# Kernel tuning notes

Measured on AMD Instinct MI355X. Metric: run time of the kernel, lower is better.

The kernel has to match this reference:

```python
import jax, jax.numpy as jnp
import numpy as np

N_CODES = 4096
D = 256


def setup_inputs() -> dict:
    key = jax.random.key(0)
    k_v, k_w = jax.random.split(key)
    v = jax.random.normal(k_v, (8, 2048, D), dtype=jnp.float32)
    # Embedding init ~ N(0,1), then softmax over dim=1, then row 0 set to 1/d (empty feature)
    w = jax.random.normal(k_w, (N_CODES, D), dtype=jnp.float32)
    w = jax.nn.softmax(w, axis=1)
    w = w.at[0].set(1.0 / D)
    return {"v": v, "vectors": w}


def reference(v, vectors):
    n, d = vectors.shape
    cb = vectors[1:]  # exclude the fixed empty feature at index 0
    # ||v - c||^2 = ||v||^2 - 2 v.c + ||c||^2  (avoids [..., n, d] intermediate)
    v2 = jnp.sum(v * v, axis=-1, keepdims=True)              # [..., 1]
    c2 = jnp.sum(cb * cb, axis=-1)                           # [n-1]
    diff = v2 - 2.0 * jnp.einsum('...d,nd->...n', v, cb) + c2  # [..., n-1]
    idx = jnp.argmin(diff, axis=-1) + 1                      # [...]
    # empty-feature mask: any component differs from 1/d
    mask = jnp.any(v != (1.0 / d), axis=-1)
    idx = jnp.where(mask, idx, 0)
    out = vectors[idx]                                       # gather == onehot @ vectors
    loss = jnp.mean(jnp.square(out - jax.lax.stop_gradient(v)))
    used = jnp.array(0, dtype=jnp.int32)  # eval mode: usage pool is empty
    return out, idx, loss, used
```

## Files before the change

### kernel.cpp

```cpp
#include <hip/hip_runtime.h>
#include <hip/hip_fp16.h>
#include <math.h>
#include <stdint.h>


#define M_TOTAL 16384
#define NCODES  4096
#define D_DIM   256

#define OUT_OFF_IDX  (M_TOTAL * D_DIM)
#define OUT_OFF_LOSS (OUT_OFF_IDX + M_TOTAL)

typedef _Float16 half8 __attribute__((ext_vector_type(8)));
typedef float    float16v __attribute__((ext_vector_type(16)));

__device__ __forceinline__ void gload_lds16(const void* g, void* l) {
  __builtin_amdgcn_global_load_lds(
      (const __attribute__((address_space(1))) void*)g,
      (__attribute__((address_space(3))) void*)l, 16, 0, 0);
}

__global__ __launch_bounds__(256) void prep_kernel(
    const float* __restrict__ V, const float* __restrict__ W,
    _Float16* __restrict__ Vp, _Float16* __restrict__ Bp,
    float* __restrict__ v2, float* __restrict__ c2,
    uint64_t* __restrict__ pk)
{
  __shared__ float T[16 * 264];
  const int t = threadIdx.x;
  const int rloc = t >> 4, seg = t & 15;
  const bool isW = blockIdx.x < 256;
  const int bid2 = isW ? blockIdx.x : (blockIdx.x - 256);
  const int row = bid2 * 16 + rloc;
  const float* X = isW ? W : V;

  if (!isW && bid2 < 64) pk[bid2 * 256 + t] = ~0ULL;

  const float* src = X + (size_t)row * D_DIM + seg * 16;
  float4 x[4];
#pragma unroll
  for (int u = 0; u < 4; ++u) x[u] = ((const float4*)src)[u];
  union { half8 v; _Float16 e[8]; } uh[2], ul[2];
#pragma unroll
  for (int u = 0; u < 4; ++u) {
    float e4[4] = {x[u].x, x[u].y, x[u].z, x[u].w};
#pragma unroll
    for (int j = 0; j < 4; ++j) {
      const int e = u * 4 + j;
      float s = e4[j] * 1024.0f;
      _Float16 h = (_Float16)s;
      uh[e >> 3].e[e & 7] = h;
      ul[e >> 3].e[e & 7] = (_Float16)(s - (float)h);
    }
    *(float4*)&T[rloc * 264 + seg * 16 + u * 4] = x[u];
  }
  if (isW) {
    const int panel = row >> 5, nin = row & 31;
    _Float16* dst = Bp + ((size_t)panel * 16 + seg) * 2048 + nin * 8;
#pragma unroll
    for (int lh = 0; lh < 2; ++lh) {
      *(half8*)(dst + lh * 256)        = uh[lh].v;
      *(half8*)(dst + 1024 + lh * 256) = ul[lh].v;
    }
  } else {
    _Float16* dst = Vp + ((size_t)(row >> 5) * 16 + seg) * 1024 + (row & 31) * 8;
#pragma unroll
    for (int lh = 0; lh < 2; ++lh) {
      *(half8*)(dst + lh * 256)        = uh[lh].v;
      *(half8*)(dst + 512 + lh * 256)  = ul[lh].v;
    }
  }
  __syncthreads();
  const int half = (t >> 3) & 1, j = t & 7;
  const float* tr = &T[rloc * 264 + half * 128 + j];
  float r = __fmul_rn(tr[0], tr[0]);
#pragma unroll
  for (int i = 1; i < 16; ++i) { float e = tr[8 * i]; r = __fadd_rn(r, __fmul_rn(e, e)); }
  r = __fadd_rn(r, __shfl_xor(r, 1));
  r = __fadd_rn(r, __shfl_xor(r, 2));
  r = __fadd_rn(r, __shfl_xor(r, 4));
  r = __fadd_rn(r, __shfl_xor(r, 8));
  if ((t & 15) == 0) { if (isW) c2[row] = r; else v2[row] = r; }
}

__global__ __launch_bounds__(256, 2) void vq_mfma_kernel(
    const _Float16* __restrict__ Vp, const _Float16* __restrict__ Bp,
    const float* __restrict__ v2, const float* __restrict__ c2,
    uint64_t* __restrict__ pk)
{
  __shared__ __align__(16) char smem[77824];
  uint64_t* red2 = (uint64_t*)(smem + 73728);

  const int tid  = threadIdx.x;
  const int lane = tid & 63;
  const int wave = tid >> 6;
  const int wr = wave >> 1, wc = wave & 1;
  const int l31 = lane & 31, lhi = lane >> 5;

  const int bid = blockIdx.x;
  const int xcd  = bid & 7;
  const int seq  = bid >> 3;
  const int mblk = xcd * 8 + (seq & 7);
  const int pblk = seq >> 3;
  const int m0 = mblk * 256;
  const int n0 = pblk * 128;

  const char* gsrc[6];
  int gstr[6], dstOff[6];
#pragma unroll
  for (int j = 0; j < 6; ++j) {
    const int c = wave * 6 + j;
    dstOff[j] = c * 1024;
    if (c < 16) {
      const int p = c >> 1, pl = c & 1;
      gsrc[j] = (const char*)Vp + ((size_t)(mblk * 8 + p) * 16) * 2048 + pl * 1024 + lane * 16;
      gstr[j] = 2048;
    } else {
      const int b = c - 16, pn = b >> 1, pl = b & 1;
      gsrc[j] = (const char*)Bp + ((size_t)(pblk * 4 + pn) * 16) * 4096 + pl * 2048 + lane * 16;
      gstr[j] = 4096;
    }
  }

  auto STAGE = [&](int kb) {
#pragma unroll
    for (int j = 0; j < 6; ++j) {
      gload_lds16(gsrc[j], smem + kb * 24576 + dstOff[j]);
      gsrc[j] += gstr[j];
    }
  };

  float16v acc[4][2];
#pragma unroll
  for (int mb = 0; mb < 4; ++mb)
#pragma unroll
    for (int nb = 0; nb < 2; ++nb) acc[mb][nb] = (float16v)0.0f;

  STAGE(0);
  STAGE(1);

#pragma unroll
  for (int k = 0; k < 16; ++k) {
    if (k < 15) asm volatile("s_waitcnt vmcnt(6)" ::: "memory");
    else        asm volatile("s_waitcnt vmcnt(0)" ::: "memory");
    __builtin_amdgcn_sched_barrier(0);
    __builtin_amdgcn_s_barrier();
    __builtin_amdgcn_sched_barrier(0);
    if (k < 14) STAGE((k + 2) % 3);

    const char* Ab = smem + (k % 3) * 24576 + (wr * 4) * 2048 + lane * 16;
    const char* Bb = smem + (k % 3) * 24576 + 16384 + (wc * 2) * 2048 + lane * 16;
    half8 ah[4], al[4], bh[2], bl[2];
#pragma unroll
    for (int mb = 0; mb < 4; ++mb) {
      ah[mb] = *(const half8*)(Ab + mb * 2048);
      al[mb] = *(const half8*)(Ab + mb * 2048 + 1024);
    }
#pragma unroll
    for (int nb = 0; nb < 2; ++nb) {
      bh[nb] = *(const half8*)(Bb + nb * 2048);
      bl[nb] = *(const half8*)(Bb + nb * 2048 + 1024);
    }
#pragma unroll
    for (int nb = 0; nb < 2; ++nb)
#pragma unroll
      for (int mb = 0; mb < 4; ++mb)
        acc[mb][nb] = __builtin_amdgcn_mfma_f32_32x32x16_f16(ah[mb], bh[nb], acc[mb][nb], 0, 0, 0);
#pragma unroll
    for (int nb = 0; nb < 2; ++nb)
#pragma unroll
      for (int mb = 0; mb < 4; ++mb)
        acc[mb][nb] = __builtin_amdgcn_mfma_f32_32x32x16_f16(ah[mb], bl[nb], acc[mb][nb], 0, 0, 0);
#pragma unroll
    for (int nb = 0; nb < 2; ++nb)
#pragma unroll
      for (int mb = 0; mb < 4; ++mb)
        acc[mb][nb] = __builtin_amdgcn_mfma_f32_32x32x16_f16(al[mb], bh[nb], acc[mb][nb], 0, 0, 0);
  }
  __syncthreads();

  float c2r[2];
#pragma unroll
  for (int nb = 0; nb < 2; ++nb) c2r[nb] = c2[n0 + wc * 64 + nb * 32 + l31];

  uint64_t* wbuf = (uint64_t*)smem + wave * 1056;

#pragma unroll
  for (int mb = 0; mb < 4; ++mb) {
#pragma unroll
    for (int r = 0; r < 16; ++r) {
      const int rowin = (r & 3) + 8 * (r >> 2) + 4 * lhi;
      const float v2m = v2[m0 + wr * 128 + mb * 32 + rowin];
      uint64_t b = ~0ULL;
#pragma unroll
      for (int nb = 0; nb < 2; ++nb) {
        const int n = n0 + wc * 64 + nb * 32 + l31;
        float dot = acc[mb][nb][r] * 0x1p-20f;
        float dd  = __fadd_rn(__fsub_rn(v2m, 2.0f * dot), c2r[nb]);
        if (n == 0) dd = INFINITY;
        uint64_t p = ((uint64_t)__float_as_uint(dd) << 32) | (uint32_t)n;
        if (p < b) b = p;
      }
      wbuf[(r * 2 + lhi) * 33 + l31] = b;
    }
    {
      const int f = lane >> 1, hf = lane & 1;
      const uint64_t* rp = wbuf + f * 33 + hf * 16;
      uint64_t m = rp[0];
#pragma unroll
      for (int i = 1; i < 16; ++i) { uint64_t v = rp[i]; if (v < m) m = v; }
      uint64_t o = __shfl_xor((unsigned long long)m, 1);
      if (o < m) m = o;
      if (hf == 0) {
        const int r_ = f >> 1, lh2 = f & 1;
        const int rowin = (r_ & 3) + 8 * (r_ >> 2) + 4 * lh2;
        red2[(wr * 128 + mb * 32 + rowin) * 2 + wc] = m;
      }
    }
  }
  __syncthreads();

  uint64_t a0 = red2[tid * 2], a1 = red2[tid * 2 + 1];
  atomicMin((unsigned long long*)&pk[m0 + tid], (unsigned long long)(a0 < a1 ? a0 : a1));
}

__global__ __launch_bounds__(256) void gather_kernel(
    const float* __restrict__ V, const float* __restrict__ W,
    const uint64_t* __restrict__ pk,
    float* __restrict__ out, float* __restrict__ outIdx,
    float* __restrict__ lossPartial)
{
  const int q = blockIdx.x * 4 + (threadIdx.x >> 6);
  const int l = threadIdx.x & 63;
  const uint64_t b = pk[q];
  float4 vv = *(const float4*)(V + (size_t)q * D_DIM + l * 4);
  const float inv = 0.00390625f;
  bool ne = (vv.x != inv) | (vv.y != inv) | (vv.z != inv) | (vv.w != inv);
  const int idx = __ballot(ne) ? (int)(uint32_t)b : 0;
  float4 o4 = *(const float4*)(W + (size_t)idx * D_DIM + l * 4);
  *(float4*)(out + (size_t)q * D_DIM + l * 4) = o4;
  if (l == 0) outIdx[q] = (float)idx;
  float dx = o4.x - vv.x, dy = o4.y - vv.y, dz = o4.z - vv.z, dw = o4.w - vv.w;
  float s = dx * dx + dy * dy + dz * dz + dw * dw;
#pragma unroll
  for (int off = 32; off; off >>= 1) s += __shfl_xor(s, off);
  if (l == 0) lossPartial[q] = s;
}

__global__ __launch_bounds__(256) void finalize_kernel(
    const float* __restrict__ lossPartial, float* __restrict__ out)
{
  const int t = threadIdx.x;
  __shared__ float red[256];
  float s = 0.0f;
  for (int i = t; i < M_TOTAL; i += 256) s += lossPartial[i];
  red[t] = s;
  __syncthreads();
  for (int st = 128; st > 0; st >>= 1) {
    if (t < st) red[t] += red[t + st];
    __syncthreads();
  }
  if (t == 0) {
    out[0] = (float)((double)red[0] / (double)(M_TOTAL * D_DIM));
    out[1] = 0.0f;
  }
}

extern "C" void kernel_launch(void* const* d_in, const int* in_sizes, int n_in,
                              void* d_out, int out_size, void* d_ws, size_t ws_size,
                              hipStream_t stream) {
  const float* V = (const float*)d_in[0];
  const float* W = (const float*)d_in[1];
  float* out = (float*)d_out;

  _Float16* Vp = (_Float16*)d_out;

  char* ws = (char*)d_ws;
  _Float16* Bp  = (_Float16*)(ws);
  float*    c2  = (float*)(ws + 8388608);
  float*    v2  = (float*)(ws + 8388608 + 16384);
  uint64_t* pk  = (uint64_t*)(ws + 8388608 + 16384 + 65536);
  float* lossPartial = (float*)(ws + 8388608 + 16384 + 65536 + 131072);

  prep_kernel<<<1280, 256, 0, stream>>>(V, W, Vp, Bp, v2, c2, pk);
  vq_mfma_kernel<<<2048, 256, 0, stream>>>(Vp, Bp, v2, c2, pk);
  gather_kernel<<<M_TOTAL / 4, 256, 0, stream>>>(V, W, pk, out, out + OUT_OFF_IDX, lossPartial);
  finalize_kernel<<<1, 256, 0, stream>>>(lossPartial, out + OUT_OFF_LOSS);
}
```

Measured before the change: 199.2 us.

## Double-buffer LDS fragment reads in registers to overlap with MFMA chain

Adds a register-level ping-pong so the A/B fragments for k-step k+1 are read from LDS while the MFMAs for step k run. The global-to-LDS stage issue, wait and barrier are reordered to fit this schedule. Occupancy in launch bounds drops from 2 to 1 block per CU so the extra fragment registers fit without spilling. This trades fewer resident waves for latency hiding, and the barrier before reading buffer k+1 must still guard against a stage overwriting it.

```diff
diff --git a/kernel.cpp b/kernel.cpp
--- a/kernel.cpp
+++ b/kernel.cpp
@@ -83,7 +83,7 @@
   if ((t & 15) == 0) { if (isW) c2[row] = r; else v2[row] = r; }
 }
 
-__global__ __launch_bounds__(256, 2) void vq_mfma_kernel(
+__global__ __launch_bounds__(256, 1) void vq_mfma_kernel(
     const _Float16* __restrict__ Vp, const _Float16* __restrict__ Bp,
     const float* __restrict__ v2, const float* __restrict__ c2,
     uint64_t* __restrict__ pk)
@@ -136,46 +136,60 @@
 #pragma unroll
     for (int nb = 0; nb < 2; ++nb) acc[mb][nb] = (float16v)0.0f;
 
+  half8 ah[2][4], al[2][4], bh[2][2], bl[2][2];
+
+  auto LDREAD = [&](int kst, int pb) {
+    const char* Ab = smem + (kst % 3) * 24576 + (wr * 4) * 2048 + lane * 16;
+    const char* Bb = smem + (kst % 3) * 24576 + 16384 + (wc * 2) * 2048 + lane * 16;
+#pragma unroll
+    for (int mb = 0; mb < 4; ++mb) {
+      ah[pb][mb] = *(const half8*)(Ab + mb * 2048);
+      al[pb][mb] = *(const half8*)(Ab + mb * 2048 + 1024);
+    }
+#pragma unroll
+    for (int nb = 0; nb < 2; ++nb) {
+      bh[pb][nb] = *(const half8*)(Bb + nb * 2048);
+      bl[pb][nb] = *(const half8*)(Bb + nb * 2048 + 1024);
+    }
+  };
+
   STAGE(0);
   STAGE(1);
+  asm volatile("s_waitcnt vmcnt(6)" ::: "memory");
+  __builtin_amdgcn_sched_barrier(0);
+  __builtin_amdgcn_s_barrier();
+  __builtin_amdgcn_sched_barrier(0);
+  LDREAD(0, 0);
+  __builtin_amdgcn_sched_barrier(0);
 
 #pragma unroll
   for (int k = 0; k < 16; ++k) {
-    if (k < 15) asm volatile("s_waitcnt vmcnt(6)" ::: "memory");
-    else        asm volatile("s_waitcnt vmcnt(0)" ::: "memory");
-    __builtin_amdgcn_sched_barrier(0);
-    __builtin_amdgcn_s_barrier();
-    __builtin_amdgcn_sched_barrier(0);
-    if (k < 14) STAGE((k + 2) % 3);
-
-    const char* Ab = smem + (k % 3) * 24576 + (wr * 4) * 2048 + lane * 16;
-    const char* Bb = smem + (k % 3) * 24576 + 16384 + (wc * 2) * 2048 + lane * 16;
-    half8 ah[4], al[4], bh[2], bl[2];
-#pragma unroll
-    for (int mb = 0; mb < 4; ++mb) {
-      ah[mb] = *(const half8*)(Ab + mb * 2048);
-      al[mb] = *(const half8*)(Ab + mb * 2048 + 1024);
-    }
-#pragma unroll
-    for (int nb = 0; nb < 2; ++nb) {
-      bh[nb] = *(const half8*)(Bb + nb * 2048);
-      bl[nb] = *(const half8*)(Bb + nb * 2048 + 1024);
+    const int pb = k & 1;
+    if (k <= 13) STAGE((k + 2) % 3);
+    if (k <= 13)      asm volatile("s_waitcnt vmcnt(6)" ::: "memory");
+    else if (k == 14) asm volatile("s_waitcnt vmcnt(0)" ::: "memory");
+    if (k < 15) {
+      __builtin_amdgcn_sched_barrier(0);
+      __builtin_amdgcn_s_barrier();
+      __builtin_amdgcn_sched_barrier(0);
+      LDREAD(k + 1, pb ^ 1);
+      __builtin_amdgcn_sched_barrier(0);
     }
 #pragma unroll
     for (int nb = 0; nb < 2; ++nb)
 #pragma unroll
       for (int mb = 0; mb < 4; ++mb)
-        acc[mb][nb] = __builtin_amdgcn_mfma_f32_32x32x16_f16(ah[mb], bh[nb], acc[mb][nb], 0, 0, 0);
+        acc[mb][nb] = __builtin_amdgcn_mfma_f32_32x32x16_f16(ah[pb][mb], bh[pb][nb], acc[mb][nb], 0, 0, 0);
 #pragma unroll
     for (int nb = 0; nb < 2; ++nb)
 #pragma unroll
       for (int mb = 0; mb < 4; ++mb)
-        acc[mb][nb] = __builtin_amdgcn_mfma_f32_32x32x16_f16(ah[mb], bl[nb], acc[mb][nb], 0, 0, 0);
+        acc[mb][nb] = __builtin_amdgcn_mfma_f32_32x32x16_f16(ah[pb][mb], bl[pb][nb], acc[mb][nb], 0, 0, 0);
 #pragma unroll
     for (int nb = 0; nb < 2; ++nb)
 #pragma unroll
       for (int mb = 0; mb < 4; ++mb)
-        acc[mb][nb] = __builtin_amdgcn_mfma_f32_32x32x16_f16(al[mb], bh[nb], acc[mb][nb], 0, 0, 0);
+        acc[mb][nb] = __builtin_amdgcn_mfma_f32_32x32x16_f16(al[pb][mb], bh[pb][nb], acc[mb][nb], 0, 0, 0);
   }
   __syncthreads();
 
```

After: 204.8 us. 2.8% more time.

## Interleave LDS reads, async global loads and MFMA phases with priority hints

Applied to the files above, without the earlier changes.

Restructures the main k-loop so LDS fragment reads, async global-to-LDS staging and the three MFMA groups run in three interleaved phases instead of loading everything up front. The barrier moves to the end of each iteration, and s_setprio raises wave priority around the MFMA bursts. The aim is to hide LDS and global load latency behind matrix math and to keep the MFMA unit busy across waves. It adds extra lgkmcnt waits and scheduling barriers, which could serialize work if the phases are too small.

```diff
diff --git a/kernel.cpp b/kernel.cpp
--- a/kernel.cpp
+++ b/kernel.cpp
@@ -122,10 +122,17 @@
     }
   }
 
-  auto STAGE = [&](int kb) {
+  auto STAGE2 = [&](int kst, int j0) {
+#pragma unroll
+    for (int j = j0; j < j0 + 2; ++j) {
+      gload_lds16(gsrc[j], smem + (kst % 3) * 24576 + dstOff[j]);
+      gsrc[j] += gstr[j];
+    }
+  };
+  auto STAGEFULL = [&](int kst) {
 #pragma unroll
     for (int j = 0; j < 6; ++j) {
-      gload_lds16(gsrc[j], smem + kb * 24576 + dstOff[j]);
+      gload_lds16(gsrc[j], smem + (kst % 3) * 24576 + dstOff[j]);
       gsrc[j] += gstr[j];
     }
   };
@@ -136,46 +143,70 @@
 #pragma unroll
     for (int nb = 0; nb < 2; ++nb) acc[mb][nb] = (float16v)0.0f;
 
-  STAGE(0);
-  STAGE(1);
+  STAGEFULL(0);
+  STAGEFULL(1);
+  asm volatile("s_waitcnt vmcnt(6)" ::: "memory");
+  __builtin_amdgcn_sched_barrier(0);
+  __builtin_amdgcn_s_barrier();
+  __builtin_amdgcn_sched_barrier(0);
 
 #pragma unroll
   for (int k = 0; k < 16; ++k) {
-    if (k < 15) asm volatile("s_waitcnt vmcnt(6)" ::: "memory");
-    else        asm volatile("s_waitcnt vmcnt(0)" ::: "memory");
-    __builtin_amdgcn_sched_barrier(0);
-    __builtin_amdgcn_s_barrier();
-    __builtin_amdgcn_sched_barrier(0);
-    if (k < 14) STAGE((k + 2) % 3);
-
     const char* Ab = smem + (k % 3) * 24576 + (wr * 4) * 2048 + lane * 16;
     const char* Bb = smem + (k % 3) * 24576 + 16384 + (wc * 2) * 2048 + lane * 16;
     half8 ah[4], al[4], bh[2], bl[2];
-#pragma unroll
-    for (int mb = 0; mb < 4; ++mb) {
-      ah[mb] = *(const half8*)(Ab + mb * 2048);
-      al[mb] = *(const half8*)(Ab + mb * 2048 + 1024);
-    }
-#pragma unroll
-    for (int nb = 0; nb < 2; ++nb) {
-      bh[nb] = *(const half8*)(Bb + nb * 2048);
-      bl[nb] = *(const half8*)(Bb + nb * 2048 + 1024);
-    }
+
+#pragma unroll
+    for (int mb = 0; mb < 4; ++mb) ah[mb] = *(const half8*)(Ab + mb * 2048);
+#pragma unroll
+    for (int nb = 0; nb < 2; ++nb) bh[nb] = *(const half8*)(Bb + nb * 2048);
+    if (k <= 13) STAGE2(k + 2, 0);
+    asm volatile("s_waitcnt lgkmcnt(0)" ::: "memory");
+    __builtin_amdgcn_sched_barrier(0);
+    __builtin_amdgcn_s_setprio(1);
 #pragma unroll
     for (int nb = 0; nb < 2; ++nb)
 #pragma unroll
       for (int mb = 0; mb < 4; ++mb)
         acc[mb][nb] = __builtin_amdgcn_mfma_f32_32x32x16_f16(ah[mb], bh[nb], acc[mb][nb], 0, 0, 0);
+    __builtin_amdgcn_s_setprio(0);
+    __builtin_amdgcn_sched_barrier(0);
+
+#pragma unroll
+    for (int nb = 0; nb < 2; ++nb) bl[nb] = *(const half8*)(Bb + nb * 2048 + 1024);
+    if (k <= 13) STAGE2(k + 2, 2);
+    asm volatile("s_waitcnt lgkmcnt(0)" ::: "memory");
+    __builtin_amdgcn_sched_barrier(0);
+    __builtin_amdgcn_s_setprio(1);
 #pragma unroll
     for (int nb = 0; nb < 2; ++nb)
 #pragma unroll
       for (int mb = 0; mb < 4; ++mb)
         acc[mb][nb] = __builtin_amdgcn_mfma_f32_32x32x16_f16(ah[mb], bl[nb], acc[mb][nb], 0, 0, 0);
+    __builtin_amdgcn_s_setprio(0);
+    __builtin_amdgcn_sched_barrier(0);
+
+#pragma unroll
+    for (int mb = 0; mb < 4; ++mb) al[mb] = *(const half8*)(Ab + mb * 2048 + 1024);
+    if (k <= 13) STAGE2(k + 2, 4);
+    asm volatile("s_waitcnt lgkmcnt(0)" ::: "memory");
+    __builtin_amdgcn_sched_barrier(0);
+    __builtin_amdgcn_s_setprio(1);
 #pragma unroll
     for (int nb = 0; nb < 2; ++nb)
 #pragma unroll
       for (int mb = 0; mb < 4; ++mb)
         acc[mb][nb] = __builtin_amdgcn_mfma_f32_32x32x16_f16(al[mb], bh[nb], acc[mb][nb], 0, 0, 0);
+    __builtin_amdgcn_s_setprio(0);
+    __builtin_amdgcn_sched_barrier(0);
+
+    if (k <= 13)      asm volatile("s_waitcnt vmcnt(6)" ::: "memory");
+    else if (k == 14) asm volatile("s_waitcnt vmcnt(0)" ::: "memory");
+    if (k < 15) {
+      __builtin_amdgcn_sched_barrier(0);
+      __builtin_amdgcn_s_barrier();
+      __builtin_amdgcn_sched_barrier(0);
+    }
   }
   __syncthreads();
 
```

Measured after the change: 192.5 us. 3.4% less time.
